# Optimization experiments

Hardware: AMD Instinct MI355X
Metric: run time of the kernel (lower is better)

Reference implementation:

```python
import jax, jax.numpy as jnp
import numpy as np

SHOT, WAY, DIM, Q, R = 5, 32, 640, 4096, 10
TEMP, L, DIV = 16.0, 2.0, 10.0
EPS = 1e-5


def _expmap0(x, c):
    # x: (..., d); c: broadcastable to (..., 1). Exponential map at origin + ball projection.
    sc = jnp.sqrt(c)
    n = jnp.maximum(jnp.linalg.norm(x, axis=-1, keepdims=True), EPS)
    y = jnp.tanh(sc * n) * x / (sc * n)
    ny = jnp.maximum(jnp.linalg.norm(y, axis=-1, keepdims=True), EPS)
    maxn = (1.0 - 1e-3) / sc
    return jnp.where(ny > maxn, y * (maxn / ny), y)


def _dist(x, y, c):
    # Poincare distance: 2/sqrt(c) * artanh(sqrt(c) * ||mobius_add(-x, y)||)
    u = -x
    uy = jnp.sum(u * y, -1, keepdims=True)
    u2 = jnp.sum(u * u, -1, keepdims=True)
    y2 = jnp.sum(y * y, -1, keepdims=True)
    num = (1.0 + 2.0 * c * uy + c * y2) * u + (1.0 - c * u2) * y
    den = jnp.maximum(1.0 + 2.0 * c * uy + c * c * u2 * y2, EPS)
    n = jnp.linalg.norm(num / den, axis=-1, keepdims=True)
    sc = jnp.sqrt(c)
    arg = jnp.clip(sc * n, 0.0, 1.0 - EPS)
    return ((2.0 / sc) * jnp.arctanh(arg))[..., 0]


def setup_inputs() -> dict:
    key = jax.random.key(0)
    ks = jax.random.split(key, 8)
    f = lambda k, s: jax.random.normal(k, s, dtype=jnp.float32)
    z = lambda s: jnp.zeros(s, jnp.float32)
    return {
        "data_shot": f(ks[0], (SHOT * WAY, DIM)),
        "data_query": f(ks[1], (Q, DIM)),
        "W1": f(ks[2], (2 * DIM, 128)) * 0.05, "b1": z((128,)),
        "W2": f(ks[3], (128, 64)) * 0.05, "b2": z((64,)),
        "W3": f(ks[4], (64, 5)) * 0.05, "b3": z((5,)),
        "Wr1": f(ks[5], (2 * R + 2, R)) * 0.05, "br1": z((R,)),
        "Wr2": f(ks[6], (R, R + 1)) * 0.05, "br2": z((R + 1,)),
    }


def reference(data_shot, data_query, W1, b1, W2, b2, W3, b3, Wr1, br1, Wr2, br2):
    # --- episode stats + per-class curvature controller ---
    all_data = jnp.concatenate([data_shot, data_query], 0).mean(0)      # (dim,)
    protos = data_shot.reshape(SHOT, WAY, DIM).mean(0)                  # (way, dim)
    ctrl_in = jnp.concatenate([protos, jnp.broadcast_to(all_data, (WAY, DIM))], 1)
    h = jax.nn.relu(ctrl_in @ W1 + b1)
    h = jax.nn.relu(h @ W2 + b2)
    cand = jnp.arange(1, 6, dtype=jnp.float32) * (L / DIV)              # 5 curvature candidates
    c = jax.nn.softmax(h @ W3 + b3, axis=-1) @ cand                     # (way,) positive curvature

    # --- hyperbolic projection + per-class proto-query distances (vectorized over classes) ---
    proto_p = _expmap0(protos, c[:, None])                              # (way, dim)
    query_p = _expmap0(data_query[None], c[:, None, None])              # (way, Q, dim)
    dis_mat = _dist(proto_p[:, None, :], query_p, c[:, None, None])     # (way, Q)

    # --- sort + gather-based rerank features ---
    idx = jnp.argsort(dis_mat, axis=1)
    idx_near, idx_far = idx[:, :R], idx[:, R:]
    n_i_d = jnp.take_along_axis(dis_mat, idx_near, 1)                   # (way, R)
    o_i_d = jnp.take_along_axis(dis_mat, idx_far, 1).mean(1)            # (way,)
    dT = dis_mat.T                                                      # (Q, way)
    Gnear = dT[idx_near]                                                # (way, R, way): [i,k,j] = dis_mat[j, idx_near[i,k]]
    n_o_d = (Gnear.sum(-1) - n_i_d) / (WAY - 1)                         # (way, R)
    Gfar = dT[idx_far]                                                  # (way, Q-R, way)
    ii = jnp.arange(WAY)
    mlt = (ii[None, :] < ii[:, None]).astype(dis_mat.dtype)             # j < i
    mgt = (ii[None, :] > ii[:, None]).astype(dis_mat.dtype)             # j > i
    sumA = jnp.einsum('ikj,ij->i', Gfar, mlt)                           # gathered cols (rows before i)
    sumB = mgt @ dis_mat[:, R:].sum(1)                                  # raw cols R: (rows after i, as in source)
    o_o_d = (sumA + sumB) / ((WAY - 1) * (Q - R))

    # --- rerank controller MLP ---
    rr_in = jnp.concatenate([n_i_d, n_o_d, o_i_d[:, None], o_o_d[:, None]], 1)  # (way, 2R+2)
    hr = jax.nn.relu(rr_in @ Wr1 + br1)
    orr = hr @ Wr2 + br2                                                # (way, R+1)
    i_w = jax.nn.softmax(orr[:, :R], axis=-1)                           # (way, R)
    onw = jax.nn.sigmoid(orr[:, R])                                     # (way,)

    # --- proto update + final distances ---
    near_q = data_query[idx_near]                                       # (way, R, dim)
    wdq = (near_q * i_w[:, :, None]).sum(1)                             # (way, dim)
    tmp = protos * onw[:, None] + wdq * (1.0 - onw[:, None])
    test_proto = _expmap0(tmp, c[:, None])
    new_dis = _dist(test_proto[:, None, :], query_p, c[:, None, None])  # (way, Q)
    return -new_dis.T / TEMP                                            # (Q, way)
```

## Files before the change

kernel.cpp:

```cpp
#include <hip/hip_runtime.h>
#include <math.h>

#define NSHOT 5
#define WAY 32
#define DIM 640
#define NQ 4096
#define RNEAR 10

constexpr int OFF_PROTOS = 0;
constexpr int OFF_QPART  = 20480;
constexpr int OFF_C      = 102400;
constexpr int OFF_BETA   = 102432;
constexpr int OFF_S      = 102464;
constexpr int OFF_U      = 102496;
constexpr int OFF_NID    = 102528;
constexpr int OFF_RR     = 102848;
constexpr int OFF_SPC    = 103552;
constexpr int OFF_H1P    = 103584;
constexpr int OFF_TP     = 107680;
constexpr int OFF_G      = 128160;
constexpr int OFF_NIDX   = 259232;
constexpr int OFF_Q2D    = 259556;
constexpr int OFF_X2D    = 267748;
constexpr int OFF_X2D2   = 267812;
constexpr int OFF_P2RAW  = 267876;
constexpr int OFF_H1PART = 268000;

__device__ __forceinline__ double wave_sum_d(double v) {
#pragma unroll
  for (int o = 32; o > 0; o >>= 1) v += __shfl_down(v, o, 64);
  return v;
}

__device__ __forceinline__ double dist_hyp(double c, double xdotq, double u2, double q2) {
  const double EPSd = 1e-5;
  double sc = sqrt(c);
  double nq = sqrt(q2);
  double nf = fmax(nq, EPSd);
  double th = tanh(sc * nf);
  double al = th / (sc * nf);
  double ny = fmax(al * nq, EPSd);
  double mx = 0.999 / sc;
  if (ny > mx) al *= mx / ny;
  double y2 = al * al * q2;
  double uy = -al * xdotq;
  double A = 1.0 + 2.0 * c * uy + c * y2;
  double B = 1.0 - c * u2;
  double den = fmax(1.0 + 2.0 * c * uy + c * c * u2 * y2, EPSd);
  double num2 = fmax(A * A * u2 + 2.0 * A * B * uy + B * B * y2, 0.0);
  double n = sqrt(num2) / den;
  double arg = sc * n;
  const double CLIP = (double)(1.0f - 1e-5f);
  arg = fmin(fmax(arg, 0.0), CLIP);
  return (1.0 / sc) * log((1.0 + arg) / (1.0 - arg));
}

__device__ __forceinline__ float dist_f32(float c, float xdotq, float u2, float q2) {
  const float EPSf = 1e-5f;
  float sc = sqrtf(c);
  float nq = sqrtf(q2);
  float nf = fmaxf(nq, EPSf);
  float th = tanhf(sc * nf);
  float al = th / (sc * nf);
  float ny = fmaxf(al * nq, EPSf);
  float mx = 0.999f / sc;
  if (ny > mx) al *= mx / ny;
  float y2 = al * al * q2;
  float uy = -al * xdotq;
  float A = 1.f + 2.f * c * uy + c * y2;
  float B = 1.f - c * u2;
  float den = fmaxf(1.f + 2.f * c * uy + c * c * u2 * y2, EPSf);
  float num2 = fmaxf(A * A * u2 + 2.f * A * B * uy + B * B * y2, 0.f);
  float n = sqrtf(num2) / den;
  float arg = sc * n;
  arg = fminf(fmaxf(arg, 0.f), 1.f - 1e-5f);
  return (1.f / sc) * logf((1.f + arg) / (1.f - arg));
}

__device__ __forceinline__ double expmap_scale(double c, double p2, double* u2out) {
  double sc = sqrt(c);
  double ntrue = sqrt(p2);
  double nf = fmax(ntrue, 1e-5);
  double th = tanh(sc * nf);
  double s0 = th / (sc * nf);
  double ny = fmax(s0 * ntrue, 1e-5);
  double mx = 0.999 / sc;
  if (ny > mx) s0 *= mx / ny;
  *u2out = s0 * s0 * p2;
  return s0;
}

__global__ __launch_bounds__(640) void k_fuse1(const float* __restrict__ Qm,
                                               const float* __restrict__ shot,
                                               const float* __restrict__ W1, float* ws) {
  __shared__ double q2w[32][10];
  __shared__ double psred[10];
  __shared__ float pr[DIM];
  __shared__ float h1pp[5][128];
  int b = blockIdx.x, t = threadIdx.x;
  int lane = t & 63, wid = t >> 6;
  float protoval = 0.f;
  if (b < WAY) {
    float s = 0.f;
#pragma unroll
    for (int s5 = 0; s5 < NSHOT; ++s5) s += shot[(size_t)(s5 * WAY + b) * DIM + t];
    protoval = s * 0.2f;
    pr[t] = protoval;
    ws[OFF_PROTOS + b * DIM + t] = protoval;
    double pv2 = (double)protoval * protoval;
    pv2 = wave_sum_d(pv2);
    if (lane == 0) psred[wid] = pv2;
  }
  int r0 = b * 32;
  float colacc = 0.f;
  for (int r = 0; r < 32; ++r) {
    float v = Qm[(size_t)(r0 + r) * DIM + t];
    colacc += v;
    double sq = (double)v * v;
    sq = wave_sum_d(sq);
    if (lane == 0) q2w[r][wid] = sq;
  }
  ws[OFF_QPART + b * DIM + t] = colacc + 5.f * protoval;
  __syncthreads();
  if (t < 32) {
    double s = 0.0;
#pragma unroll
    for (int k = 0; k < 10; ++k) s += q2w[t][k];
    ((double*)(ws + OFF_Q2D))[r0 + t] = s;
  }
  if (b < WAY) {
    int n = t & 127, s = t >> 7;
    int k0 = s * 128;
    float acc = 0.f;
#pragma unroll 8
    for (int k = k0; k < k0 + 128; ++k) acc = fmaf(pr[k], W1[(size_t)k * 128 + n], acc);
    h1pp[s][n] = acc;
    __syncthreads();
    if (t < 128)
      ws[OFF_H1P + b * 128 + t] = h1pp[0][t] + h1pp[1][t] + h1pp[2][t] + h1pp[3][t] + h1pp[4][t];
    if (t == 0) {
      double p2 = 0.0;
#pragma unroll
      for (int k = 0; k < 10; ++k) p2 += psred[k];
      ((double*)(ws + OFF_P2RAW))[b] = p2;
    }
  }
}

__global__ __launch_bounds__(320) void k_amw1(const float* __restrict__ W1, float* ws) {
  __shared__ float part_am[4][80];
  __shared__ float am_s[80];
  __shared__ float h1part[2][128];
  int j = blockIdx.x, t = threadIdx.x;
  {
    int c = t % 80, pg = t / 80;
    const float* base = ws + OFF_QPART + j * 80 + c;
    int p0 = pg * 32;
    float a0 = 0.f, a1 = 0.f, a2 = 0.f, a3 = 0.f;
#pragma unroll 8
    for (int p = 0; p < 32; p += 4) {
      a0 += base[(size_t)(p0 + p + 0) * DIM];
      a1 += base[(size_t)(p0 + p + 1) * DIM];
      a2 += base[(size_t)(p0 + p + 2) * DIM];
      a3 += base[(size_t)(p0 + p + 3) * DIM];
    }
    part_am[pg][c] = (a0 + a1) + (a2 + a3);
  }
  __syncthreads();
  if (t < 80)
    am_s[t] = (part_am[0][t] + part_am[1][t] + part_am[2][t] + part_am[3][t]) * (1.f / 4256.f);
  __syncthreads();
  if (t < 256) {
    int n = t & 127, kh = t >> 7;
    int kbase = j * 80 + kh * 40;
    float acc = 0.f;
#pragma unroll 8
    for (int k = 0; k < 40; ++k)
      acc = fmaf(am_s[kh * 40 + k], W1[(size_t)(DIM + kbase + k) * 128 + n], acc);
    h1part[kh][n] = acc;
  }
  __syncthreads();
  if (t < 128) ws[OFF_H1PART + j * 128 + t] = h1part[0][t] + h1part[1][t];
}

__global__ __launch_bounds__(128) void k_ctrl2(const float* __restrict__ b1,
                                               const float* __restrict__ W2, const float* __restrict__ b2,
                                               const float* __restrict__ W3, const float* __restrict__ b3,
                                               float* ws) {
  __shared__ float h1s[128];
  __shared__ float h2p[2][64];
  __shared__ float h2s[64], lg[5];
  int w = blockIdx.x, t = threadIdx.x;
  {
    float a = ws[OFF_H1P + w * 128 + t] + b1[t];
#pragma unroll
    for (int j = 0; j < 8; ++j) a += ws[OFF_H1PART + j * 128 + t];
    h1s[t] = fmaxf(a, 0.f);
  }
  __syncthreads();
  {
    int n = t & 63, kh = t >> 6;
    int k0 = kh * 64;
    float acc = 0.f;
#pragma unroll 8
    for (int k = 0; k < 64; ++k)
      acc = fmaf(h1s[k0 + k], W2[(size_t)(k0 + k) * 64 + n], acc);
    h2p[kh][n] = acc;
  }
  __syncthreads();
  if (t < 64) h2s[t] = fmaxf(h2p[0][t] + h2p[1][t] + b2[t], 0.f);
  __syncthreads();
  if (t < 5) {
    float acc = b3[t];
    for (int k = 0; k < 64; ++k) acc = fmaf(h2s[k], W3[k * 5 + t], acc);
    lg[t] = acc;
  }
  __syncthreads();
  if (t == 0) {
    double m = lg[0];
    for (int i = 1; i < 5; ++i) m = fmax(m, (double)lg[i]);
    double se = 0.0, cv = 0.0;
    for (int i = 0; i < 5; ++i) { double e = exp((double)lg[i] - m); se += e; cv += e * 0.2 * (double)(i + 1); }
    double c = cv / se;
    ws[OFF_C + w] = (float)c;
    double p2 = ((const double*)(ws + OFF_P2RAW))[w];
    double u2;
    double beta = expmap_scale(c, p2, &u2);
    ws[OFF_BETA + w] = (float)beta;
    ((double*)(ws + OFF_X2D))[w] = u2;
  }
}

#define GEMM_COMPUTE(BUF)                                             \
  {                                                                   \
    const float* qr = &S[BUF][q][0];                                  \
    const float* xr = &S[BUF][8 + w][0];                              \
    _Pragma("unroll")                                                 \
    for (int kk = 0; kk < 64; kk += 4) {                              \
      float4 qv = *(const float4*)(qr + kk);                          \
      float4 xv = *(const float4*)(xr + kk);                          \
      ax = fmaf(qv.x, xv.x, ax);                                      \
      ay = fmaf(qv.y, xv.y, ay);                                      \
      az = fmaf(qv.z, xv.z, az);                                      \
      aw = fmaf(qv.w, xv.w, aw);                                      \
    }                                                                 \
  }

__global__ __launch_bounds__(256) void k_gemm(const float* __restrict__ X, const float* __restrict__ Qm,
                                              float* __restrict__ ws, int mode, float* __restrict__ out) {
  __shared__ float S[2][40][68];
  int t = threadIdx.x;
  int q0 = blockIdx.x * 8;
  int rowA = t >> 4, quadA = t & 15;
  int rowB = (t + 256) >> 4;
  int rowC = (t + 512) >> 4;
  bool hasC = (t < 128);
  const float* srcA = (rowA < 8 ? Qm + (size_t)(q0 + rowA) * DIM : X + (size_t)(rowA - 8) * DIM) + quadA * 4;
  const float* srcB = X + (size_t)(rowB - 8) * DIM + quadA * 4;
  const float* srcC = X + (size_t)(rowC - 8) * DIM + quadA * 4;
  float4 a0 = *(const float4*)srcA;
  float4 a1 = *(const float4*)srcB;
  float4 a2 = {0.f, 0.f, 0.f, 0.f};
  if (hasC) a2 = *(const float4*)srcC;
  *(float4*)&S[0][rowA][quadA * 4] = a0;
  *(float4*)&S[0][rowB][quadA * 4] = a1;
  if (hasC) *(float4*)&S[0][rowC][quadA * 4] = a2;
  __syncthreads();
  a0 = *(const float4*)(srcA + 64);
  a1 = *(const float4*)(srcB + 64);
  if (hasC) a2 = *(const float4*)(srcC + 64);
  float4 b0 = {0.f,0.f,0.f,0.f}, b1 = b0, b2 = b0;
  int q = t & 7, w = t >> 3;
  float ax = 0.f, ay = 0.f, az = 0.f, aw = 0.f;
#pragma unroll
  for (int c = 0; c < 10; c += 2) {
    GEMM_COMPUTE(0)
    if (c + 2 < 10) {
      size_t kc = (size_t)(c + 2) * 64;
      b0 = *(const float4*)(srcA + kc);
      b1 = *(const float4*)(srcB + kc);
      if (hasC) b2 = *(const float4*)(srcC + kc);
    }
    if (c + 1 < 10) {
      *(float4*)&S[1][rowA][quadA * 4] = a0;
      *(float4*)&S[1][rowB][quadA * 4] = a1;
      if (hasC) *(float4*)&S[1][rowC][quadA * 4] = a2;
      __syncthreads();
      GEMM_COMPUTE(1)
      if (c + 3 < 10) {
        size_t kc = (size_t)(c + 3) * 64;
        a0 = *(const float4*)(srcA + kc);
        a1 = *(const float4*)(srcB + kc);
        if (hasC) a2 = *(const float4*)(srcC + kc);
      }
      if (c + 2 < 10) {
        *(float4*)&S[0][rowA][quadA * 4] = b0;
        *(float4*)&S[0][rowB][quadA * 4] = b1;
        if (hasC) *(float4*)&S[0][rowC][quadA * 4] = b2;
        __syncthreads();
      }
    }
  }
  float acc = (ax + ay) + (az + aw);
  int qq = q0 + q;
  const double* q2d = (const double*)(ws + OFF_Q2D);
  if (mode == 0) {
    const double* x2d = (const double*)(ws + OFF_X2D);
    float d = dist_f32(ws[OFF_C + w], ws[OFF_BETA + w] * acc, (float)x2d[w], (float)q2d[qq]);
    ws[OFF_G + (size_t)w * NQ + qq] = d;
  } else {
    const double* u2arr = (const double*)(ws + OFF_X2D2);
    double d = dist_hyp((double)ws[OFF_C + w], (double)acc, u2arr[w], q2d[qq]);
    out[(size_t)qq * WAY + w] = (float)(-d / 16.0);
  }
}

__global__ __launch_bounds__(1024) void k_topkA(float* __restrict__ ws) {
  __shared__ double sredS[16], sredU[16];
  __shared__ float cval[160];
  __shared__ int cidx[160];
  __shared__ float qvsh[RNEAR];
  __shared__ int qjsh[RNEAR];
  __shared__ float colsh[RNEAR][33];
  __shared__ float pcpart[RNEAR];
  int w = blockIdx.x, t = threadIdx.x;
  int lane = t & 63, wid = t >> 6;
  int* nidx = (int*)(ws + OFF_NIDX);
  const float* gb = ws + OFF_G + (size_t)w * NQ;
  float v0 = gb[t], v1 = gb[1024 + t], v2 = gb[2048 + t], v3 = gb[3072 + t];
  unsigned tk = 0;
  double s = (double)v0 + (double)v1 + (double)v2 + (double)v3;
  double u = (t < RNEAR) ? (double)v0 : 0.0;
  s = wave_sum_d(s);
  u = wave_sum_d(u);
  if (lane == 0) { sredS[wid] = s; sredU[wid] = u; }
  for (int r = 0; r < RNEAR; ++r) {
    float lv = INFINITY; int li = 0x7fffffff;
    if (!(tk & 1u) && (v0 < lv || (v0 == lv && t < li)))        { lv = v0; li = t; }
    if (!(tk & 2u) && (v1 < lv || (v1 == lv && 1024 + t < li))) { lv = v1; li = 1024 + t; }
    if (!(tk & 4u) && (v2 < lv || (v2 == lv && 2048 + t < li))) { lv = v2; li = 2048 + t; }
    if (!(tk & 8u) && (v3 < lv || (v3 == lv && 3072 + t < li))) { lv = v3; li = 3072 + t; }
#pragma unroll
    for (int o = 32; o > 0; o >>= 1) {
      float ov = __shfl_xor(lv, o, 64);
      int oi = __shfl_xor(li, o, 64);
      if (ov < lv || (ov == lv && oi < li)) { lv = ov; li = oi; }
    }
    if (lane == 0) { cval[wid * RNEAR + r] = lv; cidx[wid * RNEAR + r] = li; }
    if ((li & 1023) == t) tk |= 1u << (li >> 10);
  }
  __syncthreads();
  if (t == 0) {
    double S = 0.0, U = 0.0;
    for (int k = 0; k < 16; ++k) { S += sredS[k]; U += sredU[k]; }
    ws[OFF_S + w] = (float)S;
    ws[OFF_U + w] = (float)U;
  }
  if (t < 64) {
    float c0 = cval[t], c1 = cval[t + 64];
    int i0 = cidx[t], i1 = cidx[t + 64];
    float c2 = (t < 32) ? cval[t + 128] : INFINITY;
    int i2 = (t < 32) ? cidx[t + 128] : 0x7fffffff;
    unsigned m = 0;
    for (int r = 0; r < RNEAR; ++r) {
      float lv = INFINITY; int li = 0x7fffffff;
      if (!(m & 1u) && (c0 < lv || (c0 == lv && i0 < li))) { lv = c0; li = i0; }
      if (!(m & 2u) && (c1 < lv || (c1 == lv && i1 < li))) { lv = c1; li = i1; }
      if (!(m & 4u) && (c2 < lv || (c2 == lv && i2 < li))) { lv = c2; li = i2; }
#pragma unroll
      for (int o = 32; o > 0; o >>= 1) {
        float ov = __shfl_xor(lv, o, 64);
        int oi = __shfl_xor(li, o, 64);
        if (ov < lv || (ov == lv && oi < li)) { lv = ov; li = oi; }
      }
      if (lane == 0) { qvsh[r] = lv; qjsh[r] = li; }
      if (i0 == li) m |= 1u;
      if (i1 == li) m |= 2u;
      if (i2 == li) m |= 4u;
    }
  }
  __syncthreads();
  if (t < WAY * RNEAR) {
    int j = t >> 5, w2 = t & 31;
    colsh[j][w2] = ws[OFF_G + (size_t)w2 * NQ + qjsh[j]];
  }
  __syncthreads();
  if (t < RNEAR) {
    double cs = 0.0, pc = 0.0;
    for (int w2 = 0; w2 < WAY; ++w2) {
      float dv = colsh[t][w2];
      cs += dv;
      if (w2 < w) pc += dv;
    }
    ws[OFF_RR + w * 22 + t] = qvsh[t];
    ws[OFF_RR + w * 22 + RNEAR + t] = (float)((cs - qvsh[t]) / (double)(WAY - 1));
    ws[OFF_NID + w * RNEAR + t] = qvsh[t];
    nidx[w * RNEAR + t] = qjsh[t];
    pcpart[t] = (float)pc;
  }
  __syncthreads();
  if (t == 0) {
    double spc = 0.0, sn = 0.0;
    for (int j = 0; j < RNEAR; ++j) { spc += pcpart[j]; sn += qvsh[j]; }
    double S = (double)ws[OFF_S + w];
    ws[OFF_RR + w * 22 + 20] = (float)((S - sn) / (double)(NQ - RNEAR));
    ws[OFF_SPC + w] = (float)spc;
  }
}

__global__ __launch_bounds__(640) void k_refB(const float* __restrict__ Qm,
                                              const float* __restrict__ Wr1, const float* __restrict__ br1,
                                              const float* __restrict__ Wr2, const float* __restrict__ br2,
                                              float* __restrict__ ws) {
  __shared__ float Ssh[WAY], Ush[WAY];
  __shared__ float rrl[22];
  __shared__ int qj[RNEAR];
  __shared__ float hr[RNEAR], orsh[11], iw[RNEAR];
  __shared__ float onw_sh;
  __shared__ double p2red[10];
  __shared__ double gshd;
  int w = blockIdx.x, t = threadIdx.x;
  int lane = t & 63, wid = t >> 6;
  const int* nidx = (const int*)(ws + OFF_NIDX);
  if (t < WAY) { Ssh[t] = ws[OFF_S + t]; Ush[t] = ws[OFF_U + t]; }
  if (t >= 64 && t < 64 + 22) rrl[t - 64] = ws[OFF_RR + w * 22 + (t - 64)];
  if (t >= 96 && t < 96 + RNEAR) qj[t - 96] = nidx[w * RNEAR + (t - 96)];
  __syncthreads();
  if (t == 0) {
    double pref = 0.0, suf = 0.0;
    for (int j = 0; j < w; ++j) pref += (double)Ssh[j];
    for (int j = w + 1; j < WAY; ++j) suf += (double)Ssh[j] - (double)Ush[j];
    double spc = (double)ws[OFF_SPC + w];
    rrl[21] = (float)((pref - spc + suf) / ((double)(WAY - 1) * (double)(NQ - RNEAR)));
  }
  __syncthreads();
  if (t < RNEAR) {
    float a = br1[t];
    for (int k = 0; k < 22; ++k) a = fmaf(rrl[k], Wr1[k * RNEAR + t], a);
    hr[t] = fmaxf(a, 0.f);
  }
  __syncthreads();
  if (t < 11) {
    float a = br2[t];
    for (int k = 0; k < RNEAR; ++k) a = fmaf(hr[k], Wr2[k * 11 + t], a);
    orsh[t] = a;
  }
  __syncthreads();
  if (t == 0) {
    double m = orsh[0];
    for (int i = 1; i < RNEAR; ++i) m = fmax(m, (double)orsh[i]);
    double se = 0.0; double e[RNEAR];
    for (int i = 0; i < RNEAR; ++i) { e[i] = exp((double)orsh[i] - m); se += e[i]; }
    for (int i = 0; i < RNEAR; ++i) iw[i] = (float)(e[i] / se);
    onw_sh = (float)(1.0 / (1.0 + exp(-(double)orsh[10])));
  }
  __syncthreads();
  float onwv = onw_sh;
  float wd = 0.f;
#pragma unroll
  for (int j = 0; j < RNEAR; ++j)
    wd = fmaf(Qm[(size_t)qj[j] * DIM + t], iw[j], wd);
  float a0 = ws[OFF_PROTOS + w * DIM + t] * onwv + wd * (1.f - onwv);
  double ls = (double)a0 * a0;
  ls = wave_sum_d(ls);
  if (lane == 0) p2red[wid] = ls;
  __syncthreads();
  if (t == 0) {
    double p2 = 0.0;
#pragma unroll
    for (int k = 0; k < 10; ++k) p2 += p2red[k];
    double u22;
    gshd = expmap_scale((double)ws[OFF_C + w], p2, &u22);
    ((double*)(ws + OFF_X2D2))[w] = u22;
  }
  __syncthreads();
  ws[OFF_TP + w * DIM + t] = (float)gshd * a0;
}

extern "C" void kernel_launch(void* const* d_in, const int* in_sizes, int n_in,
                              void* d_out, int out_size, void* d_ws, size_t ws_size,
                              hipStream_t stream) {
  (void)in_sizes; (void)n_in; (void)out_size; (void)ws_size;
  const float* shot = (const float*)d_in[0];
  const float* qry  = (const float*)d_in[1];
  const float* W1   = (const float*)d_in[2];
  const float* b1   = (const float*)d_in[3];
  const float* W2   = (const float*)d_in[4];
  const float* b2   = (const float*)d_in[5];
  const float* W3   = (const float*)d_in[6];
  const float* b3   = (const float*)d_in[7];
  const float* Wr1  = (const float*)d_in[8];
  const float* br1  = (const float*)d_in[9];
  const float* Wr2  = (const float*)d_in[10];
  const float* br2  = (const float*)d_in[11];
  float* ws = (float*)d_ws;
  float* out = (float*)d_out;

  hipLaunchKernelGGL(k_fuse1, dim3(128), dim3(640), 0, stream, qry, shot, W1, ws);
  hipLaunchKernelGGL(k_amw1,  dim3(8), dim3(320), 0, stream, W1, ws);
  hipLaunchKernelGGL(k_ctrl2, dim3(32), dim3(128), 0, stream, b1, W2, b2, W3, b3, ws);
  hipLaunchKernelGGL(k_gemm,  dim3(512), dim3(256), 0, stream, ws + OFF_PROTOS, qry, ws, 0, out);
  hipLaunchKernelGGL(k_topkA, dim3(32), dim3(1024), 0, stream, ws);
  hipLaunchKernelGGL(k_refB,  dim3(32), dim3(640), 0, stream, qry, Wr1, br1, Wr2, br2, ws);
  hipLaunchKernelGGL(k_gemm,  dim3(512), dim3(256), 0, stream, ws + OFF_TP, qry, ws, 1, out);
}
```

Before: 81.63 us.

## Double GEMM query tile per block and compute two ways per thread

Each block of the distance GEMM now covers 16 queries instead of 8. Each thread accumulates two prototype rows against one query row, so every query load from shared memory is reused twice and the 32 prototype rows staged per block are amortized over twice as many queries. The grid shrinks from 512 to 256 blocks, which lowers occupancy and parallelism on a GPU with many CUs. Register use per thread rises.

New measurement: 80.92 us. About the same (-0.9%).

```diff
diff --git a/kernel.cpp b/kernel.cpp
--- a/kernel.cpp
+++ b/kernel.cpp
@@ -231,87 +231,94 @@
   }
 }
 
-#define GEMM_COMPUTE(BUF)                                             \
+#define GEMM_COMPUTE2(BUF)                                            \
   {                                                                   \
     const float* qr = &S[BUF][q][0];                                  \
-    const float* xr = &S[BUF][8 + w][0];                              \
+    const float* x0r = &S[BUF][16 + w0][0];                           \
+    const float* x1r = &S[BUF][16 + w1][0];                           \
     _Pragma("unroll")                                                 \
     for (int kk = 0; kk < 64; kk += 4) {                              \
       float4 qv = *(const float4*)(qr + kk);                          \
-      float4 xv = *(const float4*)(xr + kk);                          \
-      ax = fmaf(qv.x, xv.x, ax);                                      \
-      ay = fmaf(qv.y, xv.y, ay);                                      \
-      az = fmaf(qv.z, xv.z, az);                                      \
-      aw = fmaf(qv.w, xv.w, aw);                                      \
+      float4 x0v = *(const float4*)(x0r + kk);                        \
+      float4 x1v = *(const float4*)(x1r + kk);                       \
+      c0x = fmaf(qv.x, x0v.x, c0x); c0y = fmaf(qv.y, x0v.y, c0y);     \
+      c0z = fmaf(qv.z, x0v.z, c0z); c0w = fmaf(qv.w, x0v.w, c0w);     \
+      c1x = fmaf(qv.x, x1v.x, c1x); c1y = fmaf(qv.y, x1v.y, c1y);     \
+      c1z = fmaf(qv.z, x1v.z, c1z); c1w = fmaf(qv.w, x1v.w, c1w);     \
     }                                                                 \
   }
 
 __global__ __launch_bounds__(256) void k_gemm(const float* __restrict__ X, const float* __restrict__ Qm,
                                               float* __restrict__ ws, int mode, float* __restrict__ out) {
-  __shared__ float S[2][40][68];
+  __shared__ float S[2][48][68];
   int t = threadIdx.x;
-  int q0 = blockIdx.x * 8;
-  int rowA = t >> 4, quadA = t & 15;
-  int rowB = (t + 256) >> 4;
-  int rowC = (t + 512) >> 4;
-  bool hasC = (t < 128);
-  const float* srcA = (rowA < 8 ? Qm + (size_t)(q0 + rowA) * DIM : X + (size_t)(rowA - 8) * DIM) + quadA * 4;
-  const float* srcB = X + (size_t)(rowB - 8) * DIM + quadA * 4;
-  const float* srcC = X + (size_t)(rowC - 8) * DIM + quadA * 4;
+  int q0 = blockIdx.x * 16;
+  int rr = t >> 4, qd = t & 15;
+  const float* srcA = Qm + (size_t)(q0 + rr) * DIM + qd * 4;
+  const float* srcB = X + (size_t)rr * DIM + qd * 4;
+  const float* srcC = X + (size_t)(rr + 16) * DIM + qd * 4;
   float4 a0 = *(const float4*)srcA;
   float4 a1 = *(const float4*)srcB;
-  float4 a2 = {0.f, 0.f, 0.f, 0.f};
-  if (hasC) a2 = *(const float4*)srcC;
-  *(float4*)&S[0][rowA][quadA * 4] = a0;
-  *(float4*)&S[0][rowB][quadA * 4] = a1;
-  if (hasC) *(float4*)&S[0][rowC][quadA * 4] = a2;
+  float4 a2 = *(const float4*)srcC;
+  *(float4*)&S[0][rr][qd * 4] = a0;
+  *(float4*)&S[0][16 + rr][qd * 4] = a1;
+  *(float4*)&S[0][32 + rr][qd * 4] = a2;
   __syncthreads();
   a0 = *(const float4*)(srcA + 64);
   a1 = *(const float4*)(srcB + 64);
-  if (hasC) a2 = *(const float4*)(srcC + 64);
+  a2 = *(const float4*)(srcC + 64);
   float4 b0 = {0.f,0.f,0.f,0.f}, b1 = b0, b2 = b0;
-  int q = t & 7, w = t >> 3;
-  float ax = 0.f, ay = 0.f, az = 0.f, aw = 0.f;
+  int q = t & 15, wp = t >> 4;
+  int w0 = wp * 2, w1 = wp * 2 + 1;
+  float c0x = 0.f, c0y = 0.f, c0z = 0.f, c0w = 0.f;
+  float c1x = 0.f, c1y = 0.f, c1z = 0.f, c1w = 0.f;
 #pragma unroll
   for (int c = 0; c < 10; c += 2) {
-    GEMM_COMPUTE(0)
+    GEMM_COMPUTE2(0)
     if (c + 2 < 10) {
       size_t kc = (size_t)(c + 2) * 64;
       b0 = *(const float4*)(srcA + kc);
       b1 = *(const float4*)(srcB + kc);
-      if (hasC) b2 = *(const float4*)(srcC + kc);
+      b2 = *(const float4*)(srcC + kc);
     }
     if (c + 1 < 10) {
-      *(float4*)&S[1][rowA][quadA * 4] = a0;
-      *(float4*)&S[1][rowB][quadA * 4] = a1;
-      if (hasC) *(float4*)&S[1][rowC][quadA * 4] = a2;
+      *(float4*)&S[1][rr][qd * 4] = a0;
+      *(float4*)&S[1][16 + rr][qd * 4] = a1;
+      *(float4*)&S[1][32 + rr][qd * 4] = a2;
       __syncthreads();
-      GEMM_COMPUTE(1)
+      GEMM_COMPUTE2(1)
       if (c + 3 < 10) {
         size_t kc = (size_t)(c + 3) * 64;
         a0 = *(const float4*)(srcA + kc);
         a1 = *(const float4*)(srcB + kc);
-        if (hasC) a2 = *(const float4*)(srcC + kc);
+        a2 = *(const float4*)(srcC + kc);
       }
       if (c + 2 < 10) {
-        *(float4*)&S[0][rowA][quadA * 4] = b0;
-        *(float4*)&S[0][rowB][quadA * 4] = b1;
-        if (hasC) *(float4*)&S[0][rowC][quadA * 4] = b2;
+        *(float4*)&S[0][rr][qd * 4] = b0;
+        *(float4*)&S[0][16 + rr][qd * 4] = b1;
+        *(float4*)&S[0][32 + rr][qd * 4] = b2;
         __syncthreads();
       }
     }
   }
-  float acc = (ax + ay) + (az + aw);
+  float acc0 = (c0x + c0y) + (c0z + c0w);
+  float acc1 = (c1x + c1y) + (c1z + c1w);
   int qq = q0 + q;
   const double* q2d = (const double*)(ws + OFF_Q2D);
   if (mode == 0) {
     const double* x2d = (const double*)(ws + OFF_X2D);
-    float d = dist_f32(ws[OFF_C + w], ws[OFF_BETA + w] * acc, (float)x2d[w], (float)q2d[qq]);
-    ws[OFF_G + (size_t)w * NQ + qq] = d;
+    float q2f = (float)q2d[qq];
+    float d0 = dist_f32(ws[OFF_C + w0], ws[OFF_BETA + w0] * acc0, (float)x2d[w0], q2f);
+    float d1 = dist_f32(ws[OFF_C + w1], ws[OFF_BETA + w1] * acc1, (float)x2d[w1], q2f);
+    ws[OFF_G + (size_t)w0 * NQ + qq] = d0;
+    ws[OFF_G + (size_t)w1 * NQ + qq] = d1;
   } else {
     const double* u2arr = (const double*)(ws + OFF_X2D2);
-    double d = dist_hyp((double)ws[OFF_C + w], (double)acc, u2arr[w], q2d[qq]);
-    out[(size_t)qq * WAY + w] = (float)(-d / 16.0);
+    double q2 = q2d[qq];
+    double d0 = dist_hyp((double)ws[OFF_C + w0], (double)acc0, u2arr[w0], q2);
+    double d1 = dist_hyp((double)ws[OFF_C + w1], (double)acc1, u2arr[w1], q2);
+    out[(size_t)qq * WAY + w0] = (float)(-d0 / 16.0);
+    out[(size_t)qq * WAY + w1] = (float)(-d1 / 16.0);
   }
 }
 
@@ -499,8 +506,8 @@
   hipLaunchKernelGGL(k_fuse1, dim3(128), dim3(640), 0, stream, qry, shot, W1, ws);
   hipLaunchKernelGGL(k_amw1,  dim3(8), dim3(320), 0, stream, W1, ws);
   hipLaunchKernelGGL(k_ctrl2, dim3(32), dim3(128), 0, stream, b1, W2, b2, W3, b3, ws);
-  hipLaunchKernelGGL(k_gemm,  dim3(512), dim3(256), 0, stream, ws + OFF_PROTOS, qry, ws, 0, out);
+  hipLaunchKernelGGL(k_gemm,  dim3(256), dim3(256), 0, stream, ws + OFF_PROTOS, qry, ws, 0, out);
   hipLaunchKernelGGL(k_topkA, dim3(32), dim3(1024), 0, stream, ws);
   hipLaunchKernelGGL(k_refB,  dim3(32), dim3(640), 0, stream, qry, Wr1, br1, Wr2, br2, ws);
-  hipLaunchKernelGGL(k_gemm,  dim3(512), dim3(256), 0, stream, ws + OFF_TP, qry, ws, 1, out);
-}
+  hipLaunchKernelGGL(k_gemm,  dim3(256), dim3(256), 0, stream, ws + OFF_TP, qry, ws, 1, out);
+}
```
